# Kernel optimization log

Measured on AMD Instinct MI355X. Metric: run time of the kernel, lower is better.

Reference implementation:

```python
import jax, jax.numpy as jnp
import numpy as np

N = 8192
EPS = 1e-8
RADIUS2 = 0.05 ** 2  # squared neighborhood radius


def setup_inputs() -> dict:
    key = jax.random.key(0)
    ks = jax.random.split(key, 6)
    points = jax.random.uniform(ks[0], (N, 3), dtype=jnp.float32)
    seg_probs = jax.random.uniform(ks[1], (N, 3), dtype=jnp.float32)
    boundary_mask = jax.random.randint(ks[2], (N,), 0, 2) > 0
    head_mask = jax.random.randint(ks[3], (N,), 0, 2) > 0
    pred_mask = jax.random.randint(ks[4], (N,), 0, 2) > 0
    gt_mask = jax.random.randint(ks[5], (N,), 0, 2) > 0
    return {"points": points, "seg_probs": seg_probs,
            "boundary_mask": boundary_mask, "head_mask": head_mask,
            "pred_mask": pred_mask, "gt_mask": gt_mask}


def _ellipsoid_shape_loss(points, mask):
    # masked mean / covariance over head-region points, then eigen ratios
    m = mask.astype(points.dtype)[:, None]  # [N,1]
    n = jnp.sum(m)
    center = jnp.sum(points * m, axis=0) / n
    centered = (points - center) * m  # zero out non-head rows
    cov = centered.T @ centered / n  # [3,3]
    w = jnp.linalg.eigvalsh(cov)  # ascending
    a, b, c = w[2], w[1], w[0]  # descending
    loss = (b / (a + EPS) - 1.0) ** 2 + (c / (a + EPS) - 1.0) ** 2
    return jnp.where(n >= 10, loss, 0.0)


def _size_consistency_loss(pred_mask, gt_mask):
    pv = jnp.sum(pred_mask.astype(jnp.float32))
    gv = jnp.sum(gt_mask.astype(jnp.float32))
    volume_loss = (pv - gv) ** 2
    rel = jnp.abs(pv - gv) / jnp.where(gv > 0, gv, 1.0)
    return jnp.where(gv > 0, volume_loss + 0.5 * rel, volume_loss)


def _surface_smoothness_loss(points, bmask, seg_probs):
    # fused pairwise-distance + masked unbiased variance (replaces O(N) python loop)
    bf = bmask.astype(points.dtype)
    x = seg_probs[:, 2]  # head probability channel
    sq = jnp.sum(points * points, axis=1)  # [N]
    d2 = sq[:, None] + sq[None, :] - 2.0 * (points @ points.T)  # [N,N] squared dists
    vf = (d2 < RADIUS2).astype(points.dtype) * bf[:, None] * bf[None, :]  # valid pairs
    cnt = jnp.sum(vf, axis=1)  # neighbors per boundary point (incl. self)
    sx = vf @ x
    sx2 = vf @ (x * x)
    safe_n = jnp.maximum(cnt, 2.0)
    var = (sx2 - sx * sx / safe_n) / (safe_n - 1.0)  # unbiased, matches torch.var
    include = (cnt > 1.0) & bmask
    ni = jnp.sum(include)
    mean_var = jnp.sum(jnp.where(include, var, 0.0)) / jnp.maximum(ni, 1)
    ok = (jnp.sum(bf) >= 5) & (ni > 0)
    return jnp.where(ok, mean_var, 0.0)


def _connectivity_loss(points, hmask):
    hf = hmask.astype(points.dtype)
    n = jnp.sum(hf)
    center = jnp.sum(points * hf[:, None], axis=0) / n
    d = jnp.linalg.norm(points - center, axis=1)
    mean_d = jnp.sum(d * hf) / n
    var = jnp.sum(hf * (d - mean_d) ** 2) / (n - 1.0)  # unbiased
    maxd = jnp.max(jnp.where(hmask, d, -jnp.inf))
    return jnp.where(n >= 5, var / (maxd + EPS), 0.0)


def reference(points, seg_probs, boundary_mask, head_mask, pred_mask, gt_mask):
    total = (_ellipsoid_shape_loss(points, head_mask)
             + _size_consistency_loss(pred_mask, gt_mask)
             + _surface_smoothness_loss(points, boundary_mask, seg_probs)
             + _connectivity_loss(points, head_mask))
    return total
```

## Files before the change

kernel.cpp:

```cpp
#include <hip/hip_runtime.h>

#define EPSF 1e-8f
#define R2C  0.0025f
#define NJ   32


__device__ inline int read_mask(const void* p, int i, int isInt) {
    if (isInt) return ((const int*)p)[i] != 0;
    return ((const unsigned char*)p)[i] != 0;
}
__device__ inline float wave_sum(float v) {
    #pragma unroll
    for (int o = 32; o > 0; o >>= 1) v += __shfl_down(v, o, 64);
    return v;
}
__device__ inline float wave_max(float v) {
    #pragma unroll
    for (int o = 32; o > 0; o >>= 1) v = fmaxf(v, __shfl_down(v, o, 64));
    return v;
}

__global__ __launch_bounds__(256, 4)
void k_pairs(const float* __restrict__ pts, const float* __restrict__ segp,
             const void* bm, const void* hm, const void* pm, const void* gm,
             float* __restrict__ ws, int n, int nbi) {
    __shared__ float4 t4[256];
    __shared__ float2 tv[256];
    __shared__ int bad[4];
    __shared__ int wc[4];
    __shared__ float pacc[13];
    int tid = threadIdx.x, lane = tid & 63, wv = tid >> 6;
    int bx = blockIdx.x, c = blockIdx.y;

    if (tid < 4) { bad[tid] = 0; wc[tid] = 0; }
    if (tid < 13) pacc[tid] = 0.f;
    __syncthreads();
    {
        unsigned w0 = ((const unsigned*)bm)[tid & 255];
        if (w0 & 0xFFFFFF00u) atomicOr(&bad[0], 1);
        if (c == 0) {
            unsigned w1 = ((const unsigned*)hm)[tid & 255];
            unsigned w2 = ((const unsigned*)pm)[tid & 255];
            unsigned w3 = ((const unsigned*)gm)[tid & 255];
            if (w1 & 0xFFFFFF00u) atomicOr(&bad[1], 1);
            if (w2 & 0xFFFFFF00u) atomicOr(&bad[2], 1);
            if (w3 & 0xFFFFFF00u) atomicOr(&bad[3], 1);
        }
    }
    __syncthreads();

    int i0 = bx*512 + tid, i1 = i0 + 256;
    int ic0 = min(i0, n-1), ic1 = min(i1, n-1);
    bool a0 = i0 < n, a1 = i1 < n;
    float x0 = pts[3*ic0], y0 = pts[3*ic0+1], z0 = pts[3*ic0+2];
    float x1 = pts[3*ic1], y1 = pts[3*ic1+1], z1 = pts[3*ic1+2];
    int b0 = read_mask(bm, ic0, !bad[0]) && a0;
    int b1 = read_mask(bm, ic1, !bad[0]) && a1;
    float thr0 = b0 ? R2C - (x0*x0 + y0*y0 + z0*z0) : -1e30f;
    float thr1 = b1 ? R2C - (x1*x1 + y1*y1 + z1*z1) : -1e30f;

    if (c == 0) {
        int h0 = read_mask(hm, ic0, !bad[1]) && a0;
        int h1 = read_mask(hm, ic1, !bad[1]) && a1;
        int p0 = read_mask(pm, ic0, !bad[2]) && a0;
        int p1 = read_mask(pm, ic1, !bad[2]) && a1;
        int g0 = read_mask(gm, ic0, !bad[3]) && a0;
        int g1 = read_mask(gm, ic1, !bad[3]) && a1;
        float hf0 = h0 ? 1.f : 0.f, hf1 = h1 ? 1.f : 0.f;
        float vals[13] = {
            hf0*x0 + hf1*x1, hf0*y0 + hf1*y1, hf0*z0 + hf1*z1,
            hf0 + hf1, (float)(p0 + p1), (float)(g0 + g1), (float)(b0 + b1),
            hf0*x0*x0 + hf1*x1*x1, hf0*x0*y0 + hf1*x1*y1, hf0*x0*z0 + hf1*x1*z1,
            hf0*y0*y0 + hf1*y1*y1, hf0*y0*z0 + hf1*y1*z1, hf0*z0*z0 + hf1*z1*z1 };
        #pragma unroll
        for (int k = 0; k < 13; ++k) {
            float s = wave_sum(vals[k]);
            if (lane == 0) atomicAdd(&pacc[k], s);
        }
        __syncthreads();
        if (tid < 13) ws[64 + bx*16 + tid] = pacc[tid];
    }

    {
        int j = c*256 + tid;
        int jc = min(j, n-1);
        bool jb = (j < n) && read_mask(bm, jc, !bad[0]);
        float xj = pts[3*jc], yj = pts[3*jc+1], zj = pts[3*jc+2];
        float v = segp[3*jc+2];
        float sqj = xj*xj + yj*yj + zj*zj;
        unsigned long long ball = __ballot(jb);
        int pre = __popcll(ball & ((1ull << lane) - 1ull));
        if (lane == 0) wc[wv] = __popcll(ball);
        __syncthreads();
        int base = 0;
        #pragma unroll
        for (int w = 0; w < 4; ++w) base += (w < wv) ? wc[w] : 0;
        if (jb) {
            int r = base + pre;
            t4[r] = make_float4(-2.f*xj, -2.f*yj, -2.f*zj, sqj);
            tv[r] = make_float2(v, v*v);
        }
    }
    __syncthreads();
    int JC = wc[0] + wc[1] + wc[2] + wc[3];

    float c0a = 0.f, s10 = 0.f, s20 = 0.f;
    float c1a = 0.f, s11 = 0.f, s21 = 0.f;
    #pragma unroll 4
    for (int k = 0; k < JC; ++k) {
        float4 pj = t4[k];
        float2 vv = tv[k];
        float t0 = fmaf(pj.x, x0, pj.w);
        t0 = fmaf(pj.y, y0, t0);
        t0 = fmaf(pj.z, z0, t0);
        float m0 = (t0 < thr0) ? 1.f : 0.f;
        c0a += m0;
        s10 = fmaf(m0, vv.x, s10);
        s20 = fmaf(m0, vv.y, s20);
        float t1 = fmaf(pj.x, x1, pj.w);
        t1 = fmaf(pj.y, y1, t1);
        t1 = fmaf(pj.z, z1, t1);
        float m1 = (t1 < thr1) ? 1.f : 0.f;
        c1a += m1;
        s11 = fmaf(m1, vv.x, s11);
        s21 = fmaf(m1, vv.y, s21);
    }
    float* __restrict__ outb = ws + 4096;
    if (a0) {
        outb[(size_t)c*n + i0]          = c0a;
        outb[(size_t)(NJ + c)*n + i0]   = s10;
        outb[(size_t)(2*NJ + c)*n + i0] = s20;
    }
    if (a1) {
        outb[(size_t)c*n + i1]          = c1a;
        outb[(size_t)(NJ + c)*n + i1]   = s11;
        outb[(size_t)(2*NJ + c)*n + i1] = s21;
    }
}

__global__ void k_final(const float* __restrict__ pts, const void* bm, const void* hm,
                        float* __restrict__ ws, float* __restrict__ out,
                        int n, int nbi, int nsl) {
    __shared__ int badb, badh, lastf, bmax;
    __shared__ float ctr[13];
    __shared__ float bacc[4];
    int tid = threadIdx.x, lane = tid & 63;
    if (tid == 0) { badb = 0; badh = 0; lastf = 0; bmax = 0; }
    if (tid < 4) bacc[tid] = 0.f;
    __syncthreads();
    unsigned wb = ((const unsigned*)bm)[tid & 255];
    unsigned wh = ((const unsigned*)hm)[tid & 255];
    if (wb & 0xFFFFFF00u) atomicOr(&badb, 1);
    if (wh & 0xFFFFFF00u) atomicOr(&badh, 1);

    if (tid < 64) {
        float s[13] = {0,0,0,0,0,0,0,0,0,0,0,0,0};
        for (int r = tid; r < nsl; r += 64) {
            #pragma unroll
            for (int k = 0; k < 13; ++k) s[k] += ws[64 + r*16 + k];
        }
        #pragma unroll
        for (int k = 0; k < 13; ++k) {
            #pragma unroll
            for (int o = 32; o > 0; o >>= 1) s[k] += __shfl_down(s[k], o, 64);
        }
        if (tid == 0) {
            #pragma unroll
            for (int k = 0; k < 13; ++k) ctr[k] = s[k];
        }
    }
    __syncthreads();

    float nh = ctr[3];
    float inv = (nh > 0.f) ? 1.f/nh : 0.f;
    float cx = ctr[0]*inv, cy = ctr[1]*inv, cz = ctr[2]*inv;
    int i = blockIdx.x*256 + tid;
    int ic = min(i, n-1);
    float act = (i < n) ? 1.f : 0.f;
    float x = pts[3*ic], y = pts[3*ic+1], z = pts[3*ic+2];
    int h = read_mask(hm, ic, !badh);
    float m = (h ? 1.f : 0.f) * act;
    float dx = x-cx, dy = y-cy, dz = z-cz;
    float d = sqrtf(dx*dx + dy*dy + dz*dz);
    {
        float s0 = wave_sum(m*d);
        float s1 = wave_sum(m*d*d);
        float dm = wave_max(m > 0.f ? d : 0.f);
        if (lane == 0) {
            atomicAdd(&bacc[0], s0); atomicAdd(&bacc[1], s1);
            atomicMax(&bmax, __float_as_int(dm));
        }
    }
    const float* __restrict__ outb = ws + 4096;
    float sv = 0.f, nv = 0.f;
    if (i < n) {
        float c0 = 0.f, a1 = 0.f, a2 = 0.f;
        #pragma unroll
        for (int k = 0; k < NJ; ++k) {
            c0 += outb[(size_t)k*n + i];
            a1 += outb[(size_t)(NJ + k)*n + i];
            a2 += outb[(size_t)(2*NJ + k)*n + i];
        }
        int b = read_mask(bm, i, !badb);
        float safe_n = fmaxf(c0, 2.f);
        float var = (a2 - a1*a1/safe_n) / (safe_n - 1.f);
        if (b && c0 > 1.f) { sv = var; nv = 1.f; }
    }
    sv = wave_sum(sv); nv = wave_sum(nv);
    if (lane == 0) { atomicAdd(&bacc[2], sv); atomicAdd(&bacc[3], nv); }
    __syncthreads();

    float* row = ws + 1024 + blockIdx.x*16;
    if (tid < 5) {
        float val = (tid == 2) ? __int_as_float(bmax)
                  : (tid < 2 ? bacc[tid] : bacc[tid - 1]);
        atomicExch((int*)&row[tid], __float_as_int(val));
    }
    if (tid == 0) {
        __threadfence();
        unsigned prev = atomicAdd((unsigned*)ws, 1u);
        if (prev % (unsigned)gridDim.x == (unsigned)gridDim.x - 1u) lastf = 1;
    }
    __syncthreads();
    if (!lastf) return;

    if (tid < 4) bacc[tid] = 0.f;
    if (tid == 0) bmax = 0;
    __syncthreads();
    for (int t = tid; t < nbi*5; t += 256) {
        int r = t / 5, col = t % 5;
        int bits = atomicOr((int*)&ws[1024 + r*16 + col], 0);
        if (col == 2) atomicMax(&bmax, bits);
        else {
            int dst = (col < 2) ? col : col - 1;
            atomicAdd(&bacc[dst], __int_as_float(bits));
        }
    }
    __syncthreads();
    if (tid != 0) return;

    float sd = bacc[0], sd2 = bacc[1], svv = bacc[2], niv = bacc[3];
    float maxd = __int_as_float(bmax);
    float pv = ctr[4], gv = ctr[5], nbm = ctr[6];

    float el = 0.0f;
    if (nh >= 10.0f) {
        double nn  = (double)nh;
        double cxd = (double)ctr[0]/nn, cyd = (double)ctr[1]/nn, czd = (double)ctr[2]/nn;
        double axx = (double)ctr[7]/nn  - cxd*cxd;
        double axy = (double)ctr[8]/nn  - cxd*cyd;
        double axz = (double)ctr[9]/nn  - cxd*czd;
        double ayy = (double)ctr[10]/nn - cyd*cyd;
        double ayz = (double)ctr[11]/nn - cyd*czd;
        double azz = (double)ctr[12]/nn - czd*czd;
        double p1 = axy*axy + axz*axz + ayz*ayz;
        double q  = (axx + ayy + azz) / 3.0;
        double p2 = (axx-q)*(axx-q) + (ayy-q)*(ayy-q) + (azz-q)*(azz-q) + 2.0*p1;
        double e0, e2;
        if (p2 < 1e-300) { e0 = e2 = q; }
        else {
            double p = sqrt(p2 / 6.0);
            double bxx = (axx-q)/p, byy = (ayy-q)/p, bzz = (azz-q)/p;
            double bxy = axy/p, bxz = axz/p, byz = ayz/p;
            double detB = bxx*(byy*bzz - byz*byz) - bxy*(bxy*bzz - byz*bxz)
                        + bxz*(bxy*byz - byy*bxz);
            double r2 = fmin(1.0, fmax(-1.0, detB * 0.5));
            double phi = acos(r2) / 3.0;
            e2 = q + 2.0*p*cos(phi);
            e0 = q + 2.0*p*cos(phi + 2.0943951023931953);
        }
        double e1 = 3.0*q - e2 - e0;
        double ra = e1/(e2 + (double)EPSF) - 1.0;
        double rc = e0/(e2 + (double)EPSF) - 1.0;
        el = (float)(ra*ra + rc*rc);
    }
    float diff = pv - gv;
    float vol = diff * diff;
    float rel = fabsf(diff) / (gv > 0.0f ? gv : 1.0f);
    float sc = (gv > 0.0f) ? vol + 0.5f*rel : vol;
    float mean_var = svv / fmaxf(niv, 1.0f);
    float ss = ((nbm >= 5.0f) && (niv > 0.0f)) ? mean_var : 0.0f;
    float conn = 0.0f;
    if (nh >= 5.0f) {
        float var = (sd2 - sd*sd/nh) / (nh - 1.0f);
        conn = var / (maxd + EPSF);
    }
    out[0] = el + sc + ss + conn;
}

extern "C" void kernel_launch(void* const* d_in, const int* in_sizes, int n_in,
                              void* d_out, int out_size, void* d_ws, size_t ws_size,
                              hipStream_t stream) {
    const float* points = (const float*)d_in[0];
    const float* segp   = (const float*)d_in[1];
    const void*  bmask  = d_in[2];
    const void*  hmask  = d_in[3];
    const void*  pmask  = d_in[4];
    const void*  gmask  = d_in[5];
    float* ws  = (float*)d_ws;
    float* out = (float*)d_out;
    int n = in_sizes[2];
    int nbi = (n + 255) / 256;
    int nsl = (n + 511) / 512;

    k_pairs<<<dim3(nsl, NJ), 256, 0, stream>>>(points, segp, bmask, hmask,
                                               pmask, gmask, ws, n, nbi);
    k_final<<<nbi, 256, 0, stream>>>(points, bmask, hmask, ws, out, n, nbi, nsl);
}
```

Measured before the change: 26.10 us.

## Compact boundary i-points in shared memory to skip non-boundary pair work

The pair kernel now builds a compacted list of boundary i-points per block using ballots, then each thread loops over compacted entries, so non-boundary rows no longer do the inner j-loop. The final kernel skips reading the partial sums for non-boundary points. This halves pair work for a random half-density mask but adds shared memory (ci4, ilist), an extra barrier, and a loop where each thread handles one point instead of two, which lowers ILP. Unwritten workspace rows for non-boundary points are never read, so correctness holds.

```diff
diff --git a/kernel.cpp b/kernel.cpp
--- a/kernel.cpp
+++ b/kernel.cpp
@@ -26,13 +26,17 @@
              float* __restrict__ ws, int n, int nbi) {
     __shared__ float4 t4[256];
     __shared__ float2 tv[256];
+    __shared__ float4 ci4[512];
+    __shared__ short  ilist[512];
     __shared__ int bad[4];
-    __shared__ int wc[4];
+    __shared__ int wcj[4];
+    __shared__ int wci[8];
     __shared__ float pacc[13];
     int tid = threadIdx.x, lane = tid & 63, wv = tid >> 6;
     int bx = blockIdx.x, c = blockIdx.y;
 
-    if (tid < 4) { bad[tid] = 0; wc[tid] = 0; }
+    if (tid < 4) { bad[tid] = 0; wcj[tid] = 0; }
+    if (tid < 8) wci[tid] = 0;
     if (tid < 13) pacc[tid] = 0.f;
     __syncthreads();
     {
@@ -54,10 +58,8 @@
     bool a0 = i0 < n, a1 = i1 < n;
     float x0 = pts[3*ic0], y0 = pts[3*ic0+1], z0 = pts[3*ic0+2];
     float x1 = pts[3*ic1], y1 = pts[3*ic1+1], z1 = pts[3*ic1+2];
-    int b0 = read_mask(bm, ic0, !bad[0]) && a0;
-    int b1 = read_mask(bm, ic1, !bad[0]) && a1;
-    float thr0 = b0 ? R2C - (x0*x0 + y0*y0 + z0*z0) : -1e30f;
-    float thr1 = b1 ? R2C - (x1*x1 + y1*y1 + z1*z1) : -1e30f;
+    bool b0 = read_mask(bm, ic0, !bad[0]) && a0;
+    bool b1 = read_mask(bm, ic1, !bad[0]) && a1;
 
     if (c == 0) {
         int h0 = read_mask(hm, ic0, !bad[1]) && a0;
@@ -69,7 +71,8 @@
         float hf0 = h0 ? 1.f : 0.f, hf1 = h1 ? 1.f : 0.f;
         float vals[13] = {
             hf0*x0 + hf1*x1, hf0*y0 + hf1*y1, hf0*z0 + hf1*z1,
-            hf0 + hf1, (float)(p0 + p1), (float)(g0 + g1), (float)(b0 + b1),
+            hf0 + hf1, (float)(p0 + p1), (float)(g0 + g1),
+            (float)((int)b0 + (int)b1),
             hf0*x0*x0 + hf1*x1*x1, hf0*x0*y0 + hf1*x1*y1, hf0*x0*z0 + hf1*x1*z1,
             hf0*y0*y0 + hf1*y1*y1, hf0*y0*z0 + hf1*y1*z1, hf0*z0*z0 + hf1*z1*z1 };
         #pragma unroll
@@ -79,6 +82,30 @@
         }
         __syncthreads();
         if (tid < 13) ws[64 + bx*16 + tid] = pacc[tid];
+    }
+
+    {
+        unsigned long long ball0 = __ballot(b0);
+        unsigned long long ball1 = __ballot(b1);
+        if (lane == 0) { wci[wv] = __popcll(ball0); wci[4 + wv] = __popcll(ball1); }
+        __syncthreads();
+        unsigned long long lmask = (1ull << lane) - 1ull;
+        int base0 = 0, base1 = wci[0] + wci[1] + wci[2] + wci[3];
+        #pragma unroll
+        for (int w = 0; w < 4; ++w) {
+            base0 += (w < wv) ? wci[w] : 0;
+            base1 += (w < wv) ? wci[4 + w] : 0;
+        }
+        if (b0) {
+            int e = base0 + __popcll(ball0 & lmask);
+            ci4[e] = make_float4(x0, y0, z0, R2C - (x0*x0 + y0*y0 + z0*z0));
+            ilist[e] = (short)tid;
+        }
+        if (b1) {
+            int e = base1 + __popcll(ball1 & lmask);
+            ci4[e] = make_float4(x1, y1, z1, R2C - (x1*x1 + y1*y1 + z1*z1));
+            ilist[e] = (short)(tid + 256);
+        }
     }
 
     {
@@ -90,11 +117,11 @@
         float sqj = xj*xj + yj*yj + zj*zj;
         unsigned long long ball = __ballot(jb);
         int pre = __popcll(ball & ((1ull << lane) - 1ull));
-        if (lane == 0) wc[wv] = __popcll(ball);
+        if (lane == 0) wcj[wv] = __popcll(ball);
         __syncthreads();
         int base = 0;
         #pragma unroll
-        for (int w = 0; w < 4; ++w) base += (w < wv) ? wc[w] : 0;
+        for (int w = 0; w < 4; ++w) base += (w < wv) ? wcj[w] : 0;
         if (jb) {
             int r = base + pre;
             t4[r] = make_float4(-2.f*xj, -2.f*yj, -2.f*zj, sqj);
@@ -102,39 +129,30 @@
         }
     }
     __syncthreads();
-    int JC = wc[0] + wc[1] + wc[2] + wc[3];
-
-    float c0a = 0.f, s10 = 0.f, s20 = 0.f;
-    float c1a = 0.f, s11 = 0.f, s21 = 0.f;
-    #pragma unroll 4
-    for (int k = 0; k < JC; ++k) {
-        float4 pj = t4[k];
-        float2 vv = tv[k];
-        float t0 = fmaf(pj.x, x0, pj.w);
-        t0 = fmaf(pj.y, y0, t0);
-        t0 = fmaf(pj.z, z0, t0);
-        float m0 = (t0 < thr0) ? 1.f : 0.f;
-        c0a += m0;
-        s10 = fmaf(m0, vv.x, s10);
-        s20 = fmaf(m0, vv.y, s20);
-        float t1 = fmaf(pj.x, x1, pj.w);
-        t1 = fmaf(pj.y, y1, t1);
-        t1 = fmaf(pj.z, z1, t1);
-        float m1 = (t1 < thr1) ? 1.f : 0.f;
-        c1a += m1;
-        s11 = fmaf(m1, vv.x, s11);
-        s21 = fmaf(m1, vv.y, s21);
-    }
+    int JC   = wcj[0] + wcj[1] + wcj[2] + wcj[3];
+    int icnt = wci[0] + wci[1] + wci[2] + wci[3]
+             + wci[4] + wci[5] + wci[6] + wci[7];
+
     float* __restrict__ outb = ws + 4096;
-    if (a0) {
-        outb[(size_t)c*n + i0]          = c0a;
-        outb[(size_t)(NJ + c)*n + i0]   = s10;
-        outb[(size_t)(2*NJ + c)*n + i0] = s20;
-    }
-    if (a1) {
-        outb[(size_t)c*n + i1]          = c1a;
-        outb[(size_t)(NJ + c)*n + i1]   = s11;
-        outb[(size_t)(2*NJ + c)*n + i1] = s21;
+    for (int e = tid; e < icnt; e += 256) {
+        float4 ci = ci4[e];
+        float cc = 0.f, s1 = 0.f, s2 = 0.f;
+        #pragma unroll 4
+        for (int k = 0; k < JC; ++k) {
+            float4 pj = t4[k];
+            float2 vv = tv[k];
+            float t = fmaf(pj.x, ci.x, pj.w);
+            t = fmaf(pj.y, ci.y, t);
+            t = fmaf(pj.z, ci.z, t);
+            float m = (t < ci.w) ? 1.f : 0.f;
+            cc += m;
+            s1 = fmaf(m, vv.x, s1);
+            s2 = fmaf(m, vv.y, s2);
+        }
+        int i = bx*512 + (int)ilist[e];
+        outb[(size_t)c*n + i]          = cc;
+        outb[(size_t)(NJ + c)*n + i]   = s1;
+        outb[(size_t)(2*NJ + c)*n + i] = s2;
     }
 }
 
@@ -193,7 +211,8 @@
     }
     const float* __restrict__ outb = ws + 4096;
     float sv = 0.f, nv = 0.f;
-    if (i < n) {
+    bool b = (i < n) && read_mask(bm, ic, !badb);
+    if (b) {
         float c0 = 0.f, a1 = 0.f, a2 = 0.f;
         #pragma unroll
         for (int k = 0; k < NJ; ++k) {
@@ -201,10 +220,9 @@
             a1 += outb[(size_t)(NJ + k)*n + i];
             a2 += outb[(size_t)(2*NJ + k)*n + i];
         }
-        int b = read_mask(bm, i, !badb);
         float safe_n = fmaxf(c0, 2.f);
         float var = (a2 - a1*a1/safe_n) / (safe_n - 1.f);
-        if (b && c0 > 1.f) { sv = var; nv = 1.f; }
+        if (c0 > 1.f) { sv = var; nv = 1.f; }
     }
     sv = wave_sum(sv); nv = wave_sum(nv);
     if (lane == 0) { atomicAdd(&bacc[2], sv); atomicAdd(&bacc[3], nv); }
```

Result: slower. 41.15 us (+57.7%).
